# Performance work log

Hardware: AMD Instinct MI355X
Metric: run time of the kernel (lower is better)

## Reference

```python
import jax, jax.numpy as jnp
import numpy as np
import math

D_MODEL = 512
D_STATE = 16
D_CONV = 4
EXPAND = 2
D_INNER = D_MODEL * EXPAND
B, L = 2, 2048
EPS = 1e-8


def setup_inputs() -> dict:
    key = jax.random.key(0)
    ks = jax.random.split(key, 10)
    s_in = 1.0 / math.sqrt(D_MODEL)
    s_x = 1.0 / math.sqrt(D_INNER)
    s_c = 1.0 / math.sqrt(D_CONV)
    return {
        "x": jax.random.normal(ks[0], (B, L, D_MODEL), jnp.float32),
        "W_in": jax.random.uniform(ks[1], (D_MODEL, 2 * D_INNER), jnp.float32, -s_in, s_in),
        "b_in": jax.random.uniform(ks[2], (2 * D_INNER,), jnp.float32, -s_in, s_in),
        "conv_w": jax.random.uniform(ks[3], (D_INNER, 1, D_CONV), jnp.float32, -s_c, s_c),
        "conv_b": jax.random.uniform(ks[4], (D_INNER,), jnp.float32, -s_c, s_c),
        "W_x": jax.random.uniform(ks[5], (D_INNER, 2 * D_STATE + 1), jnp.float32, -s_x, s_x),
        "b_x": jax.random.uniform(ks[6], (2 * D_STATE + 1,), jnp.float32, -s_x, s_x),
        "A_log": jax.random.uniform(ks[7], (D_STATE,), jnp.float32, -math.log(D_STATE), -1.0),
        "D": jnp.ones((D_INNER,), jnp.float32),
        "W_out": jax.random.uniform(ks[8], (D_INNER, D_MODEL), jnp.float32, -s_x, s_x),
        "b_out": jax.random.uniform(ks[9], (D_MODEL,), jnp.float32, -s_x, s_x),
    }


def _silu(v):
    return v * jax.nn.sigmoid(v)


def _causal_depthwise_conv(x_blc, conv_w, conv_b):
    # x_blc: (B, L, D_inner); conv_w: (D_inner, 1, K). Torch pads K-1 both sides
    # then slices [:L] == causal left pad of K-1.
    lhs = jnp.transpose(x_blc, (0, 2, 1))  # (B, C, L)
    out = jax.lax.conv_general_dilated(
        lhs, conv_w,
        window_strides=(1,),
        padding=[(D_CONV - 1, 0)],
        dimension_numbers=("NCH", "OIH", "NCH"),
        feature_group_count=D_INNER,
    )
    out = out + conv_b[None, :, None]
    return jnp.transpose(out, (0, 2, 1))  # (B, L, C)


def reference(x, W_in, b_in, conv_w, conv_b, W_x, b_x, A_log, D, W_out, b_out):
    # in_proj and split
    xr = x @ W_in + b_in                      # (B, L, 2*Di)
    x_inner, res = jnp.split(xr, 2, axis=-1)  # each (B, L, Di)

    xc = _silu(_causal_depthwise_conv(x_inner, conv_w, conv_b))  # (B, L, Di)

    # selective scan (cumprod/cumsum formulation, faithful to source)
    BCdt = xc @ W_x + b_x                     # (B, L, 2S+1)
    B_sel = BCdt[..., :D_STATE]               # (B, L, S)
    C_sel = BCdt[..., D_STATE:2 * D_STATE]    # (B, L, S)
    dt = jax.nn.softplus(BCdt[..., -1:])      # (B, L, 1)

    A = -jnp.exp(A_log)                       # (S,)
    A_bar = jnp.exp(dt * A[None, None, :])    # (B, L, S)
    P = jnp.maximum(jnp.cumprod(A_bar, axis=1), EPS)  # (B, L, S)

    u = B_sel[..., None] * xc[:, :, None, :]  # (B, L, S, Di)
    g = jnp.cumsum(u / P[..., None], axis=1)  # (B, L, S, Di)
    h = g * P[..., None]                      # (B, L, S, Di)
    y = jnp.einsum("bls,blsd->bld", C_sel, h) + D[None, None, :] * xc

    y = y * _silu(res)
    return y @ W_out + b_out
```

## Files before the change

### kernel.cpp

```cpp
#include <hip/hip_runtime.h>
#include <hip/hip_bf16.h>
#include <cmath>


#define L_SEQ 2048
#define NBATCH 2
#define DI 1024
#define NC 64
#define LC 32
#define EPS_F 1e-8f
#define LOG_EPS -18.420680744f

typedef __attribute__((ext_vector_type(8))) __bf16 bf16x8;
typedef __attribute__((ext_vector_type(4))) float f32x4;

__device__ __forceinline__ float silu_f(float v) {
    return v / (1.f + __expf(-v));
}

__device__ __forceinline__ ushort bf16_bits(float v) {
    __hip_bfloat16 h = __float2bfloat16(v);
    return *reinterpret_cast<ushort*>(&h);
}

__device__ __forceinline__ float bf2f(ushort u) {
    union { unsigned u; float f; } c;
    c.u = ((unsigned)u) << 16;
    return c.f;
}

__global__ __launch_bounds__(256) void gemm1_mfma(
    const ushort* __restrict__ A, const ushort* __restrict__ Bt,
    const float* __restrict__ bias, ushort* __restrict__ C0,
    ushort* __restrict__ C1, int M, int N, int K)
{
    __shared__ ushort lA[128 * 64];
    __shared__ ushort lB[128 * 64];
    const int tid = threadIdx.x;
    const int w = tid >> 6, ln = tid & 63;
    const int wr = w >> 1, wc = w & 1;
    const int bm = blockIdx.y * 128, bn = blockIdx.x * 128;
    const int q = ln >> 4, r = ln & 15;
    f32x4 acc[4][4] = {};

    for (int k0 = 0; k0 < K; k0 += 64) {
        #pragma unroll
        for (int j = 0; j < 4; ++j) {
            int i = (w * 4 + j) * 64 + ln;
            int m = i >> 3, k8 = (i & 7) * 8;
            __builtin_amdgcn_global_load_lds(
                (const __attribute__((address_space(1))) void*)(A + (size_t)(bm + m) * K + k0 + k8),
                (__attribute__((address_space(3))) void*)(lA + (size_t)i * 8),
                16, 0, 0);
            __builtin_amdgcn_global_load_lds(
                (const __attribute__((address_space(1))) void*)(Bt + (size_t)(bn + m) * K + k0 + k8),
                (__attribute__((address_space(3))) void*)(lB + (size_t)i * 8),
                16, 0, 0);
        }
        __syncthreads();
        #pragma unroll
        for (int kk = 0; kk < 2; ++kk) {
            const int ko = kk * 32 + q * 8;
            bf16x8 af[4], bfr[4];
            #pragma unroll
            for (int m = 0; m < 4; ++m)
                af[m] = *reinterpret_cast<const bf16x8*>(&lA[(wr * 64 + m * 16 + r) * 64 + ko]);
            #pragma unroll
            for (int n = 0; n < 4; ++n)
                bfr[n] = *reinterpret_cast<const bf16x8*>(&lB[(wc * 64 + n * 16 + r) * 64 + ko]);
            #pragma unroll
            for (int m = 0; m < 4; ++m)
                #pragma unroll
                for (int n = 0; n < 4; ++n)
                    acc[m][n] = __builtin_amdgcn_mfma_f32_16x16x32_bf16(af[m], bfr[n], acc[m][n], 0, 0, 0);
        }
        __syncthreads();
    }

    const bool lo = (bn < 1024);
    #pragma unroll
    for (int n = 0; n < 4; ++n) {
        int col = bn + wc * 64 + n * 16 + r;
        float bv = bias[col];
        #pragma unroll
        for (int m = 0; m < 4; ++m) {
            int row0 = bm + wr * 64 + m * 16 + q * 4;
            #pragma unroll
            for (int j = 0; j < 4; ++j) {
                ushort v = bf16_bits(acc[m][n][j] + bv);
                if (lo) C0[(size_t)(row0 + j) * 1024 + col] = v;
                else    C1[(size_t)(row0 + j) * 1024 + (col - 1024)] = v;
            }
        }
    }
}

__global__ __launch_bounds__(256) void gemm2_mfma(
    const ushort* __restrict__ A, const ushort* __restrict__ Bt,
    const float* __restrict__ bias, float* __restrict__ C,
    int M, int N, int K)
{
    __shared__ ushort lA[128 * 64];
    __shared__ ushort lB[64 * 64];
    const int tid = threadIdx.x;
    const int w = tid >> 6, ln = tid & 63;
    const int wr = w >> 1, wc = w & 1;
    const int bm = blockIdx.y * 128, bn = blockIdx.x * 64;
    const int q = ln >> 4, r = ln & 15;
    f32x4 acc[4][2] = {};

    for (int k0 = 0; k0 < K; k0 += 64) {
        #pragma unroll
        for (int j = 0; j < 4; ++j) {
            int i = (w * 4 + j) * 64 + ln;
            int m = i >> 3, k8 = (i & 7) * 8;
            __builtin_amdgcn_global_load_lds(
                (const __attribute__((address_space(1))) void*)(A + (size_t)(bm + m) * K + k0 + k8),
                (__attribute__((address_space(3))) void*)(lA + (size_t)i * 8),
                16, 0, 0);
        }
        #pragma unroll
        for (int j = 0; j < 2; ++j) {
            int i = (w * 2 + j) * 64 + ln;
            int m = i >> 3, k8 = (i & 7) * 8;
            __builtin_amdgcn_global_load_lds(
                (const __attribute__((address_space(1))) void*)(Bt + (size_t)(bn + m) * K + k0 + k8),
                (__attribute__((address_space(3))) void*)(lB + (size_t)i * 8),
                16, 0, 0);
        }
        __syncthreads();
        #pragma unroll
        for (int kk = 0; kk < 2; ++kk) {
            const int ko = kk * 32 + q * 8;
            bf16x8 af[4], bfr[2];
            #pragma unroll
            for (int m = 0; m < 4; ++m)
                af[m] = *reinterpret_cast<const bf16x8*>(&lA[(wr * 64 + m * 16 + r) * 64 + ko]);
            #pragma unroll
            for (int n = 0; n < 2; ++n)
                bfr[n] = *reinterpret_cast<const bf16x8*>(&lB[(wc * 32 + n * 16 + r) * 64 + ko]);
            #pragma unroll
            for (int m = 0; m < 4; ++m)
                #pragma unroll
                for (int n = 0; n < 2; ++n)
                    acc[m][n] = __builtin_amdgcn_mfma_f32_16x16x32_bf16(af[m], bfr[n], acc[m][n], 0, 0, 0);
        }
        __syncthreads();
    }

    #pragma unroll
    for (int n = 0; n < 2; ++n) {
        int col = bn + wc * 32 + n * 16 + r;
        float bv = bias[col];
        #pragma unroll
        for (int m = 0; m < 4; ++m) {
            int row0 = bm + wr * 64 + m * 16 + q * 4;
            #pragma unroll
            for (int j = 0; j < 4; ++j)
                C[(size_t)(row0 + j) * N + col] = acc[m][n][j] + bv;
        }
    }
}

__global__ __launch_bounds__(256) void conv_gemm3(
    const ushort* __restrict__ xinb, const float* __restrict__ cw,
    const float* __restrict__ cb, const ushort* __restrict__ Wxt,
    ushort* __restrict__ xcb, float* __restrict__ P)
{
    __shared__ ushort sxin[67 * 128];
    __shared__ ushort sxc[64 * 128];
    __shared__ ushort swx[48 * 128];
    __shared__ float  scw[128][4];
    __shared__ float  scb[128];

    const int t = threadIdx.x;
    const int ks = blockIdx.x, rt = blockIdx.y;
    const int bm = rt * 64;
    const int kb = ks * 128;
    const int l0 = bm & (L_SEQ - 1);

    for (int i = t; i < 67 * 16; i += 256) {
        int rr = i >> 4, c8 = (i & 15) * 8;
        uint4 v = {0, 0, 0, 0};
        if (l0 + rr - 3 >= 0)
            v = *reinterpret_cast<const uint4*>(&xinb[(size_t)(bm + rr - 3) * 1024 + kb + c8]);
        *reinterpret_cast<uint4*>(&sxin[rr * 128 + c8]) = v;
    }
    for (int i = t; i < 48 * 16; i += 256) {
        int rr = i >> 4, c8 = (i & 15) * 8;
        *reinterpret_cast<uint4*>(&swx[rr * 128 + c8]) =
            *reinterpret_cast<const uint4*>(&Wxt[(size_t)rr * 1024 + kb + c8]);
    }
    for (int i = t; i < 512; i += 256) scw[i >> 2][i & 3] = cw[(size_t)(kb + (i >> 2)) * 4 + (i & 3)];
    if (t < 128) scb[t] = cb[kb + t];
    __syncthreads();

    for (int i = t; i < 1024; i += 256) {
        int row = i >> 4, c8 = (i & 15) * 8;
        ushort ov[8];
        #pragma unroll
        for (int j = 0; j < 8; ++j) {
            int col = c8 + j;
            float a = scb[col];
            a = fmaf(bf2f(sxin[(row + 0) * 128 + col]), scw[col][0], a);
            a = fmaf(bf2f(sxin[(row + 1) * 128 + col]), scw[col][1], a);
            a = fmaf(bf2f(sxin[(row + 2) * 128 + col]), scw[col][2], a);
            a = fmaf(bf2f(sxin[(row + 3) * 128 + col]), scw[col][3], a);
            ov[j] = bf16_bits(silu_f(a));
        }
        *reinterpret_cast<uint4*>(&sxc[row * 128 + c8]) = *reinterpret_cast<uint4*>(ov);
        *reinterpret_cast<uint4*>(&xcb[(size_t)(bm + row) * 1024 + kb + c8]) =
            *reinterpret_cast<uint4*>(ov);
    }
    __syncthreads();

    const int w = t >> 6, ln = t & 63;
    const int q = ln >> 4, r = ln & 15;
    f32x4 acc[3] = {};
    #pragma unroll
    for (int kk = 0; kk < 4; ++kk) {
        const int ko = kk * 32 + q * 8;
        bf16x8 af = *reinterpret_cast<const bf16x8*>(&sxc[(w * 16 + r) * 128 + ko]);
        #pragma unroll
        for (int n = 0; n < 3; ++n) {
            bf16x8 bf = *reinterpret_cast<const bf16x8*>(&swx[(n * 16 + r) * 128 + ko]);
            acc[n] = __builtin_amdgcn_mfma_f32_16x16x32_bf16(af, bf, acc[n], 0, 0, 0);
        }
    }

    const int row0 = bm + w * 16 + q * 4;
    const size_t base = (size_t)ks * 196608;
    #pragma unroll
    for (int n = 0; n < 3; ++n)
        #pragma unroll
        for (int j = 0; j < 4; ++j)
            P[base + (size_t)(row0 + j) * 48 + n * 16 + r] = acc[n][j];
}

__global__ __launch_bounds__(256) void gemm3_reduce(
    const float* __restrict__ P, const float* __restrict__ b_x,
    float* __restrict__ scal)
{
    int idx = blockIdx.x * 256 + threadIdx.x;
    int l = idx / 48, c = idx - l * 48;
    if (c >= 33) return;
    float v = b_x[c];
    #pragma unroll
    for (int k = 0; k < 8; ++k) v += P[idx + k * 196608];
    scal[(size_t)l * 48 + c] = v;
}

__global__ __launch_bounds__(256) void prep_all(
    const float* __restrict__ x, const float* __restrict__ W_in,
    const float* __restrict__ W_out, const float* __restrict__ W_x,
    ushort* __restrict__ xbf, ushort* __restrict__ Wt1,
    ushort* __restrict__ Wt2, ushort* __restrict__ Wxt)
{
    const int bid = blockIdx.x;
    const int t = threadIdx.x;
    if (bid < 2048) {
        int i = bid * 256 + t;
        float4 v = reinterpret_cast<const float4*>(x)[i];
        ushort4 o;
        o.x = bf16_bits(v.x); o.y = bf16_bits(v.y);
        o.z = bf16_bits(v.z); o.w = bf16_bits(v.w);
        reinterpret_cast<ushort4*>(xbf)[i] = o;
        return;
    }
    if (bid >= 2432) {
        int idx = (bid - 2432) * 256 + t;
        int c = idx >> 10, k = idx & 1023;
        Wxt[idx] = (c < 33) ? bf16_bits(W_x[(size_t)k * 33 + c]) : (ushort)0;
        return;
    }
    __shared__ float ld[64][65];
    const float* src; ushort* dst; int R, C, tile;
    if (bid < 2304) { src = W_in;  dst = Wt1; R = 512;  C = 2048; tile = bid - 2048; }
    else            { src = W_out; dst = Wt2; R = 1024; C = 512;  tile = bid - 2304; }
    const int ctiles = C / 64;
    const int r0 = (tile / ctiles) * 64, c0 = (tile % ctiles) * 64;
    #pragma unroll
    for (int i = 0; i < 16; ++i) {
        int idx = t + i * 256;
        int rr = idx >> 6, cc = idx & 63;
        ld[rr][cc] = src[(size_t)(r0 + rr) * C + c0 + cc];
    }
    __syncthreads();
    #pragma unroll
    for (int i = 0; i < 16; ++i) {
        int idx = t + i * 256;
        int cc = idx >> 6, rr = idx & 63;
        dst[(size_t)(c0 + cc) * R + r0 + rr] = bf16_bits(ld[rr][cc]);
    }
}

__global__ __launch_bounds__(256) void rates_par(
    float* __restrict__ scal, const float* __restrict__ A_log,
    float* __restrict__ RP)
{
    int b = blockIdx.x;
    int t = threadIdx.x;
    __shared__ float cdt[L_SEQ];
    __shared__ float wsum[4];
    __shared__ float An[16];
    if (t < 16) An[t] = -__expf(A_log[t]);
    float* base = scal + (long)b * L_SEQ * 48;

    float dt[8];
    float run = 0.f;
    const int l0 = t * 8;
    #pragma unroll
    for (int i = 0; i < 8; ++i) {
        float raw = base[(l0 + i) * 48 + 32];
        float d = (raw > 20.f) ? raw : log1pf(__expf(raw));
        dt[i] = d;
        run += d;
        cdt[l0 + i] = run;
    }

    float x = run;
    int lane = t & 63;
    #pragma unroll
    for (int d = 1; d < 64; d <<= 1) {
        float v = __shfl_up(x, d, 64);
        if (lane >= d) x += v;
    }
    int w = t >> 6;
    if (lane == 63) wsum[w] = x;
    __syncthreads();
    float woff = 0.f;
    for (int i = 0; i < w; ++i) woff += wsum[i];
    float toff = woff + x - run;
    #pragma unroll
    for (int i = 0; i < 8; ++i) cdt[l0 + i] += toff;
    __syncthreads();

    float cprev = (l0 == 0) ? 0.f : cdt[l0 - 1];
    #pragma unroll
    for (int i = 0; i < 8; ++i) {
        int l = l0 + i;
        float cl = cdt[l];
        float rv[16];
        #pragma unroll
        for (int s = 0; s < 16; ++s) {
            float A = An[s];
            float rr;
            if (A * cl >= LOG_EPS) {
                rr = __expf(A * dt[i]);
            } else {
                float lp = A * cprev;
                rr = (lp >= LOG_EPS) ? EPS_F / __expf(lp) : 1.f;
            }
            rv[s] = rr;
        }
        float4* dst = reinterpret_cast<float4*>(base + l * 48 + 32);
        dst[0] = *reinterpret_cast<float4*>(&rv[0]);
        dst[1] = *reinterpret_cast<float4*>(&rv[4]);
        dst[2] = *reinterpret_cast<float4*>(&rv[8]);
        dst[3] = *reinterpret_cast<float4*>(&rv[12]);
        cprev = cl;
    }

    if ((t & 3) == 3) {
        int c = t >> 2;
        float ce = cdt[c * LC + LC - 1];
        float cp = (c == 0) ? 0.f : cdt[c * LC - 1];
        for (int s = 0; s < 16; ++s) {
            float A = An[s];
            float pe = fmaxf(__expf(A * ce), EPS_F);
            float pp = fmaxf(__expf(A * cp), EPS_F);
            RP[(b * NC + c) * 16 + s] = pe / pp;
        }
    }
}

__global__ __launch_bounds__(128) void scan_states(
    const float* __restrict__ scal, const ushort* __restrict__ xcb,
    ushort* __restrict__ Sbf)
{
    int b = blockIdx.z, c = blockIdx.y;
    int d = blockIdx.x * 128 + threadIdx.x;
    __shared__ float sc[LC * 48];
    const float4* src = reinterpret_cast<const float4*>(scal + ((long)(b * L_SEQ) + c * LC) * 48);
    float4* dst = reinterpret_cast<float4*>(sc);
    for (int i = threadIdx.x; i < LC * 48 / 4; i += 128) dst[i] = src[i];

    const ushort* xcp = xcb + ((long)(b * L_SEQ) + c * LC) * 1024 + d;
    float xv[LC];
    #pragma unroll
    for (int ll = 0; ll < LC; ++ll) xv[ll] = bf2f(xcp[(long)ll * 1024]);
    __syncthreads();

    float h[16];
    #pragma unroll
    for (int s = 0; s < 16; ++s) h[s] = 0.f;
    #pragma unroll
    for (int ll = 0; ll < LC; ++ll) {
        const float* e = sc + ll * 48;
        #pragma unroll
        for (int s = 0; s < 16; ++s) h[s] = fmaf(e[32 + s], h[s], e[s] * xv[ll]);
    }
    ushort* Sp = Sbf + ((long)(b * NC + c) * 16) * 1024 + d;
    #pragma unroll
    for (int s = 0; s < 16; ++s) Sp[(long)s * 1024] = bf16_bits(h[s]);
}

__global__ __launch_bounds__(256) void stitch(
    ushort* __restrict__ Sbf, const float* __restrict__ RP)
{
    const int tid = threadIdx.x;
    const int idx = blockIdx.x * 256 + tid;
    const int b = blockIdx.y;
    const int d = idx & 1023, s = idx >> 10;
    __shared__ float rps[NC];
    if (tid < NC) rps[tid] = RP[(b * NC + tid) * 16 + s];

    const long base = ((long)(b * NC) * 16 + s) * 1024 + d;
    const long cs = 16 * 1024;
    float v[NC];
    #pragma unroll
    for (int c = 0; c < NC; ++c) v[c] = bf2f(Sbf[base + c * cs]);
    __syncthreads();
    float H = 0.f;
    #pragma unroll
    for (int c = 0; c < NC; ++c) {
        float tmp = v[c];
        v[c] = H;
        H = fmaf(rps[c], H, tmp);
    }
    #pragma unroll
    for (int c = 0; c < NC; ++c) Sbf[base + c * cs] = bf16_bits(v[c]);
}

__global__ __launch_bounds__(128) void scan_out(
    const float* __restrict__ scal, const ushort* __restrict__ xcb,
    const ushort* __restrict__ Hin, const float* __restrict__ Dw,
    const ushort* __restrict__ resb, ushort* __restrict__ ybf)
{
    int b = blockIdx.z, c = blockIdx.y;
    int d = blockIdx.x * 128 + threadIdx.x;
    __shared__ float sc[LC * 48];
    const float4* src = reinterpret_cast<const float4*>(scal + ((long)(b * L_SEQ) + c * LC) * 48);
    float4* dst = reinterpret_cast<float4*>(sc);
    for (int i = threadIdx.x; i < LC * 48 / 4; i += 128) dst[i] = src[i];

    const long row0 = (long)(b * L_SEQ) + c * LC;
    float xv[LC], rv[LC];
    #pragma unroll
    for (int ll = 0; ll < LC; ++ll) xv[ll] = bf2f(xcb[(row0 + ll) * 1024 + d]);
    #pragma unroll
    for (int ll = 0; ll < LC; ++ll) rv[ll] = bf2f(resb[(row0 + ll) * 1024 + d]);
    float h[16];
    long hoff = ((long)(b * NC + c) * 16) * 1024 + d;
    #pragma unroll
    for (int s = 0; s < 16; ++s) h[s] = bf2f(Hin[hoff + (long)s * 1024]);
    __syncthreads();

    float Dd = Dw[d];
    #pragma unroll
    for (int ll = 0; ll < LC; ++ll) {
        const float* e = sc + ll * 48;
        float y = 0.f;
        #pragma unroll
        for (int s = 0; s < 16; ++s) {
            h[s] = fmaf(e[32 + s], h[s], e[s] * xv[ll]);
            y = fmaf(e[16 + s], h[s], y);
        }
        y = fmaf(Dd, xv[ll], y);
        ybf[(row0 + ll) * 1024 + d] = bf16_bits(y * silu_f(rv[ll]));
    }
}

extern "C" void kernel_launch(void* const* d_in, const int* in_sizes, int n_in,
                              void* d_out, int out_size, void* d_ws, size_t ws_size,
                              hipStream_t stream)
{
    const float* x      = (const float*)d_in[0];
    const float* W_in   = (const float*)d_in[1];
    const float* b_in   = (const float*)d_in[2];
    const float* conv_w = (const float*)d_in[3];
    const float* conv_b = (const float*)d_in[4];
    const float* W_x    = (const float*)d_in[5];
    const float* b_x    = (const float*)d_in[6];
    const float* A_log  = (const float*)d_in[7];
    const float* Dw     = (const float*)d_in[8];
    const float* W_out  = (const float*)d_in[9];
    const float* b_out  = (const float*)d_in[10];
    float* out = (float*)d_out;

    ushort* u    = (ushort*)d_ws;
    ushort* xinb = u;
    ushort* resb = xinb + 4194304;
    ushort* xcb  = resb + 4194304;
    ushort* Sbf  = xcb + 4194304;
    ushort* xbf  = Sbf + 2097152;
    ushort* Wt1  = xbf + 2097152;
    ushort* Wt2  = Wt1 + 1048576;
    ushort* Wxt  = Wt2 + 524288;
    ushort* ybf  = Wxt + 49152;
    float* scal  = (float*)(ybf + 4194304);
    float* RP    = scal + 196608;
    float* P     = RP + 2048;

    prep_all<<<2624, 256, 0, stream>>>(x, W_in, W_out, W_x, xbf, Wt1, Wt2, Wxt);

    gemm1_mfma<<<dim3(2048 / 128, 4096 / 128), 256, 0, stream>>>(
        xbf, Wt1, b_in, xinb, resb, 4096, 2048, 512);

    conv_gemm3<<<dim3(8, 64), 256, 0, stream>>>(xinb, conv_w, conv_b, Wxt, xcb, P);

    gemm3_reduce<<<768, 256, 0, stream>>>(P, b_x, scal);

    rates_par<<<NBATCH, 256, 0, stream>>>(scal, A_log, RP);

    scan_states<<<dim3(DI / 128, NC, NBATCH), 128, 0, stream>>>(scal, xcb, Sbf);
    stitch<<<dim3(64, NBATCH), 256, 0, stream>>>(Sbf, RP);
    scan_out<<<dim3(DI / 128, NC, NBATCH), 128, 0, stream>>>(scal, xcb, Sbf, Dw, resb, ybf);

    gemm2_mfma<<<dim3(512 / 64, 4096 / 128), 256, 0, stream>>>(
        ybf, Wt2, b_out, out, 4096, 512, 1024);
}
```

Measured before the change: 109.7 us.

## Move per-state decay rate computation from serial 2-block kernel into scan kernels

The rates kernel ran with only two blocks and computed 16 exp-based decay rates per timestep, writing them into the scalar buffer. Now it only writes softplus dt and its cumulative sum. The scan_states and scan_out blocks each recompute the rates for their own chunk in shared memory. The reduce kernel also splits its output into a compact 32-wide B/C array plus a separate dt vector. This removes the low-parallelism work from the critical path, at the cost of computing the rates twice and adding a sync in each scan block.

```diff
diff --git a/kernel.cpp b/kernel.cpp
--- a/kernel.cpp
+++ b/kernel.cpp
@@ -27,6 +27,12 @@
     union { unsigned u; float f; } c;
     c.u = ((unsigned)u) << 16;
     return c.f;
+}
+
+__device__ __forceinline__ float rate_of(float A, float dl, float cl, float cp) {
+    if (A * cl >= LOG_EPS) return __expf(A * dl);
+    float lp = A * cp;
+    return (lp >= LOG_EPS) ? EPS_F / __expf(lp) : 1.f;
 }
 
 __global__ __launch_bounds__(256) void gemm1_mfma(
@@ -239,15 +245,25 @@
 
 __global__ __launch_bounds__(256) void gemm3_reduce(
     const float* __restrict__ P, const float* __restrict__ b_x,
-    float* __restrict__ scal)
-{
-    int idx = blockIdx.x * 256 + threadIdx.x;
-    int l = idx / 48, c = idx - l * 48;
-    if (c >= 33) return;
-    float v = b_x[c];
-    #pragma unroll
-    for (int k = 0; k < 8; ++k) v += P[idx + k * 196608];
-    scal[(size_t)l * 48 + c] = v;
+    float* __restrict__ scal32, float* __restrict__ dtr)
+{
+    const int bid = blockIdx.x;
+    if (bid < 512) {
+        int idx = bid * 256 + threadIdx.x;
+        int l = idx >> 5, c = idx & 31;
+        int pi = l * 48 + c;
+        float v = b_x[c];
+        #pragma unroll
+        for (int k = 0; k < 8; ++k) v += P[pi + k * 196608];
+        scal32[idx] = v;
+    } else {
+        int l = (bid - 512) * 256 + threadIdx.x;
+        int pi = l * 48 + 32;
+        float v = b_x[32];
+        #pragma unroll
+        for (int k = 0; k < 8; ++k) v += P[pi + k * 196608];
+        dtr[l] = v;
+    }
 }
 
 __global__ __launch_bounds__(256) void prep_all(
@@ -294,9 +310,9 @@
     }
 }
 
-__global__ __launch_bounds__(256) void rates_par(
-    float* __restrict__ scal, const float* __restrict__ A_log,
-    float* __restrict__ RP)
+__global__ __launch_bounds__(256) void rates_scan(
+    const float* __restrict__ dtr, const float* __restrict__ A_log,
+    float* __restrict__ dtv, float* __restrict__ dtc, float* __restrict__ RP)
 {
     int b = blockIdx.x;
     int t = threadIdx.x;
@@ -304,14 +320,14 @@
     __shared__ float wsum[4];
     __shared__ float An[16];
     if (t < 16) An[t] = -__expf(A_log[t]);
-    float* base = scal + (long)b * L_SEQ * 48;
+    const float* dr = dtr + (size_t)b * L_SEQ;
 
     float dt[8];
     float run = 0.f;
     const int l0 = t * 8;
     #pragma unroll
     for (int i = 0; i < 8; ++i) {
-        float raw = base[(l0 + i) * 48 + 32];
+        float raw = dr[l0 + i];
         float d = (raw > 20.f) ? raw : log1pf(__expf(raw));
         dt[i] = d;
         run += d;
@@ -335,31 +351,15 @@
     for (int i = 0; i < 8; ++i) cdt[l0 + i] += toff;
     __syncthreads();
 
-    float cprev = (l0 == 0) ? 0.f : cdt[l0 - 1];
-    #pragma unroll
-    for (int i = 0; i < 8; ++i) {
-        int l = l0 + i;
-        float cl = cdt[l];
-        float rv[16];
-        #pragma unroll
-        for (int s = 0; s < 16; ++s) {
-            float A = An[s];
-            float rr;
-            if (A * cl >= LOG_EPS) {
-                rr = __expf(A * dt[i]);
-            } else {
-                float lp = A * cprev;
-                rr = (lp >= LOG_EPS) ? EPS_F / __expf(lp) : 1.f;
-            }
-            rv[s] = rr;
-        }
-        float4* dst = reinterpret_cast<float4*>(base + l * 48 + 32);
-        dst[0] = *reinterpret_cast<float4*>(&rv[0]);
-        dst[1] = *reinterpret_cast<float4*>(&rv[4]);
-        dst[2] = *reinterpret_cast<float4*>(&rv[8]);
-        dst[3] = *reinterpret_cast<float4*>(&rv[12]);
-        cprev = cl;
-    }
+    float cv[8];
+    #pragma unroll
+    for (int i = 0; i < 8; ++i) cv[i] = cdt[l0 + i];
+    float4* dv = reinterpret_cast<float4*>(dtv + (size_t)b * L_SEQ + l0);
+    float4* dc = reinterpret_cast<float4*>(dtc + (size_t)b * L_SEQ + l0);
+    dv[0] = *reinterpret_cast<float4*>(&dt[0]);
+    dv[1] = *reinterpret_cast<float4*>(&dt[4]);
+    dc[0] = *reinterpret_cast<float4*>(&cv[0]);
+    dc[1] = *reinterpret_cast<float4*>(&cv[4]);
 
     if ((t & 3) == 3) {
         int c = t >> 2;
@@ -375,20 +375,40 @@
 }
 
 __global__ __launch_bounds__(128) void scan_states(
-    const float* __restrict__ scal, const ushort* __restrict__ xcb,
-    ushort* __restrict__ Sbf)
+    const float* __restrict__ scal32, const float* __restrict__ dtv,
+    const float* __restrict__ dtc, const float* __restrict__ A_log,
+    const ushort* __restrict__ xcb, ushort* __restrict__ Sbf)
 {
     int b = blockIdx.z, c = blockIdx.y;
     int d = blockIdx.x * 128 + threadIdx.x;
-    __shared__ float sc[LC * 48];
-    const float4* src = reinterpret_cast<const float4*>(scal + ((long)(b * L_SEQ) + c * LC) * 48);
-    float4* dst = reinterpret_cast<float4*>(sc);
-    for (int i = threadIdx.x; i < LC * 48 / 4; i += 128) dst[i] = src[i];
-
-    const ushort* xcp = xcb + ((long)(b * L_SEQ) + c * LC) * 1024 + d;
+    const int t = threadIdx.x;
+    __shared__ float sbc[LC * 32];
+    __shared__ float srt[LC][16];
+    __shared__ float An[16];
+
+    const float4* src = reinterpret_cast<const float4*>(scal32 + ((size_t)(b * L_SEQ) + c * LC) * 32);
+    float4* dst = reinterpret_cast<float4*>(sbc);
+    for (int i = t; i < LC * 32 / 4; i += 128) dst[i] = src[i];
+    if (t < 16) An[t] = -__expf(A_log[t]);
+
+    const ushort* xcp = xcb + ((size_t)(b * L_SEQ) + c * LC) * 1024 + d;
     float xv[LC];
     #pragma unroll
-    for (int ll = 0; ll < LC; ++ll) xv[ll] = bf2f(xcp[(long)ll * 1024]);
+    for (int ll = 0; ll < LC; ++ll) xv[ll] = bf2f(xcp[(size_t)ll * 1024]);
+    __syncthreads();
+
+    {
+        const int gb = b * L_SEQ + c * LC;
+        #pragma unroll
+        for (int k = 0; k < 4; ++k) {
+            int idx = t * 4 + k;
+            int l = idx >> 4, s = idx & 15;
+            float cl = dtc[gb + l];
+            float dl = dtv[gb + l];
+            float cp = (c == 0 && l == 0) ? 0.f : dtc[gb + l - 1];
+            srt[l][s] = rate_of(An[s], dl, cl, cp);
+        }
+    }
     __syncthreads();
 
     float h[16];
@@ -396,13 +416,13 @@
     for (int s = 0; s < 16; ++s) h[s] = 0.f;
     #pragma unroll
     for (int ll = 0; ll < LC; ++ll) {
-        const float* e = sc + ll * 48;
-        #pragma unroll
-        for (int s = 0; s < 16; ++s) h[s] = fmaf(e[32 + s], h[s], e[s] * xv[ll]);
-    }
-    ushort* Sp = Sbf + ((long)(b * NC + c) * 16) * 1024 + d;
-    #pragma unroll
-    for (int s = 0; s < 16; ++s) Sp[(long)s * 1024] = bf16_bits(h[s]);
+        const float* e = sbc + ll * 32;
+        #pragma unroll
+        for (int s = 0; s < 16; ++s) h[s] = fmaf(srt[ll][s], h[s], e[s] * xv[ll]);
+    }
+    ushort* Sp = Sbf + ((size_t)(b * NC + c) * 16) * 1024 + d;
+    #pragma unroll
+    for (int s = 0; s < 16; ++s) Sp[(size_t)s * 1024] = bf16_bits(h[s]);
 }
 
 __global__ __launch_bounds__(256) void stitch(
@@ -433,16 +453,23 @@
 }
 
 __global__ __launch_bounds__(128) void scan_out(
-    const float* __restrict__ scal, const ushort* __restrict__ xcb,
-    const ushort* __restrict__ Hin, const float* __restrict__ Dw,
-    const ushort* __restrict__ resb, ushort* __restrict__ ybf)
+    const float* __restrict__ scal32, const float* __restrict__ dtv,
+    const float* __restrict__ dtc, const float* __restrict__ A_log,
+    const ushort* __restrict__ xcb, const ushort* __restrict__ Hin,
+    const float* __restrict__ Dw, const ushort* __restrict__ resb,
+    ushort* __restrict__ ybf)
 {
     int b = blockIdx.z, c = blockIdx.y;
     int d = blockIdx.x * 128 + threadIdx.x;
-    __shared__ float sc[LC * 48];
-    const float4* src = reinterpret_cast<const float4*>(scal + ((long)(b * L_SEQ) + c * LC) * 48);
-    float4* dst = reinterpret_cast<float4*>(sc);
-    for (int i = threadIdx.x; i < LC * 48 / 4; i += 128) dst[i] = src[i];
+    const int t = threadIdx.x;
+    __shared__ float sbc[LC * 32];
+    __shared__ float srt[LC][16];
+    __shared__ float An[16];
+
+    const float4* src = reinterpret_cast<const float4*>(scal32 + ((size_t)(b * L_SEQ) + c * LC) * 32);
+    float4* dst = reinterpret_cast<float4*>(sbc);
+    for (int i = t; i < LC * 32 / 4; i += 128) dst[i] = src[i];
+    if (t < 16) An[t] = -__expf(A_log[t]);
 
     const long row0 = (long)(b * L_SEQ) + c * LC;
     float xv[LC], rv[LC];
@@ -456,14 +483,28 @@
     for (int s = 0; s < 16; ++s) h[s] = bf2f(Hin[hoff + (long)s * 1024]);
     __syncthreads();
 
+    {
+        const int gb = b * L_SEQ + c * LC;
+        #pragma unroll
+        for (int k = 0; k < 4; ++k) {
+            int idx = t * 4 + k;
+            int l = idx >> 4, s = idx & 15;
+            float cl = dtc[gb + l];
+            float dl = dtv[gb + l];
+            float cp = (c == 0 && l == 0) ? 0.f : dtc[gb + l - 1];
+            srt[l][s] = rate_of(An[s], dl, cl, cp);
+        }
+    }
+    __syncthreads();
+
     float Dd = Dw[d];
     #pragma unroll
     for (int ll = 0; ll < LC; ++ll) {
-        const float* e = sc + ll * 48;
+        const float* e = sbc + ll * 32;
         float y = 0.f;
         #pragma unroll
         for (int s = 0; s < 16; ++s) {
-            h[s] = fmaf(e[32 + s], h[s], e[s] * xv[ll]);
+            h[s] = fmaf(srt[ll][s], h[s], e[s] * xv[ll]);
             y = fmaf(e[16 + s], h[s], y);
         }
         y = fmaf(Dd, xv[ll], y);
@@ -498,8 +539,11 @@
     ushort* Wt2  = Wt1 + 1048576;
     ushort* Wxt  = Wt2 + 524288;
     ushort* ybf  = Wxt + 49152;
-    float* scal  = (float*)(ybf + 4194304);
-    float* RP    = scal + 196608;
+    float* scal32 = (float*)(ybf + 4194304);
+    float* dtr   = scal32 + 131072;
+    float* dtv   = dtr + 4096;
+    float* dtc   = dtv + 4096;
+    float* RP    = dtc + 4096;
     float* P     = RP + 2048;
 
     prep_all<<<2624, 256, 0, stream>>>(x, W_in, W_out, W_x, xbf, Wt1, Wt2, Wxt);
@@ -509,13 +553,15 @@
 
     conv_gemm3<<<dim3(8, 64), 256, 0, stream>>>(xinb, conv_w, conv_b, Wxt, xcb, P);
 
-    gemm3_reduce<<<768, 256, 0, stream>>>(P, b_x, scal);
-
-    rates_par<<<NBATCH, 256, 0, stream>>>(scal, A_log, RP);
-
-    scan_states<<<dim3(DI / 128, NC, NBATCH), 128, 0, stream>>>(scal, xcb, Sbf);
+    gemm3_reduce<<<528, 256, 0, stream>>>(P, b_x, scal32, dtr);
+
+    rates_scan<<<NBATCH, 256, 0, stream>>>(dtr, A_log, dtv, dtc, RP);
+
+    scan_states<<<dim3(DI / 128, NC, NBATCH), 128, 0, stream>>>(
+        scal32, dtv, dtc, A_log, xcb, Sbf);
     stitch<<<dim3(64, NBATCH), 256, 0, stream>>>(Sbf, RP);
-    scan_out<<<dim3(DI / 128, NC, NBATCH), 128, 0, stream>>>(scal, xcb, Sbf, Dw, resb, ybf);
+    scan_out<<<dim3(DI / 128, NC, NBATCH), 128, 0, stream>>>(
+        scal32, dtv, dtc, A_log, xcb, Sbf, Dw, resb, ybf);
 
     gemm2_mfma<<<dim3(512 / 64, 4096 / 128), 256, 0, stream>>>(
         ybf, Wt2, b_out, out, 4096, 512, 1024);
```

New measurement: 102.2 us. 1.07x faster.
